# Optimization experiments

Measured on AMD Instinct MI355X. Metric: run time of the kernel, lower is better.

## Reference

```python
import jax, jax.numpy as jnp
from jax import lax
import numpy as np

BETA = 0.5       # leak factor of snn.Leaky
THR = 1.0        # firing threshold
SLOPE = 25.0     # fast_sigmoid surrogate slope (snntorch default)
NUM_STEPS = 16

@jax.custom_vjp
def spike(m):
    # Heaviside of (mem - threshold); surrogate grad = 1/(slope*|m|+1)^2
    return (m > 0).astype(m.dtype)

def _spike_fwd(m):
    return spike(m), m

def _spike_bwd(m, g):
    return (g / (SLOPE * jnp.abs(m) + 1.0) ** 2,)

spike.defvjp(_spike_fwd, _spike_bwd)


def setup_inputs() -> dict:
    key = jax.random.key(0)
    k1, k2, k3 = jax.random.split(key, 3)
    x = jax.random.uniform(k1, (4096, 1, 28, 28), dtype=jnp.float32)
    conv_w = jax.random.normal(k2, (8, 1, 3, 3), dtype=jnp.float32) * 0.3
    fc_w = jax.random.normal(k3, (10, 1352), dtype=jnp.float32) * 0.05
    return {"x": x, "conv_w": conv_w, "fc_w": fc_w}


def reference(x, conv_w, fc_w):
    B = x.shape[0]
    # conv1(x) is identical every timestep -> compute once (same math).
    cur1 = lax.conv_general_dilated(
        x, conv_w, window_strides=(1, 1), padding='VALID',
        dimension_numbers=('NCHW', 'OIHW', 'NCHW'))  # [B,8,26,26]

    mem1_0 = jnp.zeros_like(cur1)
    mem2_0 = jnp.zeros((B, 10), dtype=x.dtype)

    def step(carry, _):
        mem1, mem2 = carry
        # LIF layer 1: integrate, fire, subtract-reset (reset detached)
        mem1 = BETA * mem1 + cur1
        spk1 = spike(mem1 - THR)
        mem1 = mem1 - lax.stop_gradient(spk1) * THR
        # avg pool 2x2 -> [B,8,13,13]
        pool = spk1.reshape(B, 8, 13, 2, 13, 2).mean(axis=(3, 5))
        # fc (no bias): [B,1352] @ [1352,10]
        cur2 = pool.reshape(B, -1) @ fc_w.T
        # LIF layer 2
        mem2 = BETA * mem2 + cur2
        spk2 = spike(mem2 - THR)
        mem2 = mem2 - lax.stop_gradient(spk2) * THR
        return (mem1, mem2), spk2

    (_, _), spk2_rec = lax.scan(step, (mem1_0, mem2_0), None, length=NUM_STEPS)
    return spk2_rec.sum(axis=0)  # [B,10] spike counts
```

## Files before the change

### kernel.cpp

```cpp
#include <hip/hip_runtime.h>


typedef float v2f __attribute__((ext_vector_type(2)));
typedef unsigned v2u __attribute__((ext_vector_type(2)));

#if __has_builtin(__builtin_elementwise_fma)
#define VFMA(a, b, c) __builtin_elementwise_fma((a), (b), (c))
#else
#define VFMA(a, b, c) ((a) * (b) + (c))
#endif

#define NU 6

__device__ __forceinline__ float bfly16(float x) {
#if __has_builtin(__builtin_amdgcn_permlane16_swap)
    v2u r = __builtin_amdgcn_permlane16_swap(__float_as_uint(x), __float_as_uint(x),
                                             false, false);
    return __uint_as_float(r.x) + __uint_as_float(r.y);
#else
    return x + __shfl_xor(x, 16);
#endif
}

__device__ __forceinline__ float pairfold16(float a, float b) {
#if __has_builtin(__builtin_amdgcn_permlane16_swap)
    v2u r = __builtin_amdgcn_permlane16_swap(__float_as_uint(a), __float_as_uint(b),
                                             false, false);
    return __uint_as_float(r.x) + __uint_as_float(r.y);
#else
    const float sa = a + __shfl_xor(a, 16);
    const float sb = b + __shfl_xor(b, 16);
    return ((threadIdx.x & 16) != 0) ? sb : sa;
#endif
}

__device__ __forceinline__ float pairfold32(float a, float b) {
#if __has_builtin(__builtin_amdgcn_permlane32_swap)
    v2u r = __builtin_amdgcn_permlane32_swap(__float_as_uint(a), __float_as_uint(b),
                                             false, false);
    return __uint_as_float(r.x) + __uint_as_float(r.y);
#else
    const float sa = a + __shfl_xor(a, 32);
    const float sb = b + __shfl_xor(b, 32);
    return ((threadIdx.x & 32) != 0) ? sb : sa;
#endif
}

template<int N>
__device__ __forceinline__ float dpp_ror_add(float x) {
#if __has_builtin(__builtin_amdgcn_update_dpp)
    int y = __builtin_amdgcn_update_dpp(0, __float_as_int(x), 0x120 + N, 0xf, 0xf, false);
    return x + __int_as_float(y);
#else
    return x + __shfl_xor(x, N);
#endif
}

__global__ __launch_bounds__(256, 3) void snn_fused_kernel(
    const float* __restrict__ x,
    const float* __restrict__ conv_w,
    const float* __restrict__ fc_w,
    float* __restrict__ out)
{
    const int b    = blockIdx.x;
    const int tid  = threadIdx.x;
    const int lane = tid & 63;
    const int wid  = tid >> 6;

    __shared__ float scw[72];
    __shared__ float sred[16 * 165];
    __shared__ float scur2[160];

    if (tid < 72) scw[tid] = conv_w[tid];

    int xbase[NU], kbase[NU];
    v2f wl[NU][5];
    #pragma unroll
    for (int i = 0; i < NU; ++i) {
        const int u      = tid + 256 * i;
        const bool valid = (u < 1352);
        const int uu  = valid ? u : 0;
        const int k   = uu / 169;
        const int rem = uu - k * 169;
        const int pr  = rem / 13;
        const int pc  = rem - pr * 13;
        xbase[i] = 56 * pr + 2 * pc;
        kbase[i] = 9 * k;
        const float sc = valid ? 0.25f : 0.0f;
        #pragma unroll
        for (int j = 0; j < 5; ++j)
            wl[i][j] = (v2f){sc * fc_w[(2 * j) * 1352 + uu],
                             sc * fc_w[(2 * j + 1) * 1352 + uu]};
    }
    __syncthreads();

    const float* xb = x + (size_t)b * 784;
    v2f cur2[NU][2];
    v2f mem2[NU][2];
    #pragma unroll
    for (int i = 0; i < NU; ++i) {
        float cw[9];
        #pragma unroll
        for (int qq = 0; qq < 9; ++qq) cw[qq] = scw[kbase[i] + qq];

        float xr[4][4];
        #pragma unroll
        for (int r = 0; r < 4; ++r) {
            const float2* rp = reinterpret_cast<const float2*>(xb + xbase[i] + 28 * r);
            const float2 a = rp[0], c2 = rp[1];
            xr[r][0] = a.x; xr[r][1] = a.y; xr[r][2] = c2.x; xr[r][3] = c2.y;
        }

        const bool valid = (tid + 256 * i) < 1352;
        float cell[2][2];
        #pragma unroll
        for (int dr = 0; dr < 2; ++dr)
            #pragma unroll
            for (int dc = 0; dc < 2; ++dc) {
                float acc = 0.0f;
                #pragma unroll
                for (int ki = 0; ki < 3; ++ki)
                    #pragma unroll
                    for (int kj = 0; kj < 3; ++kj)
                        acc += xr[dr + ki][dc + kj] * cw[ki * 3 + kj];
                cell[dr][dc] = valid ? acc : 0.0f;
            }
        cur2[i][0] = (v2f){cell[0][0], cell[0][1]};
        cur2[i][1] = (v2f){cell[1][0], cell[1][1]};
        mem2[i][0] = (v2f){0.0f, 0.0f};
        mem2[i][1] = (v2f){0.0f, 0.0f};
    }

    const v2f half2 = (v2f){0.5f, 0.5f};

    auto stageA = [&](v2f& a01, v2f& a23, v2f& a45, v2f& a67, v2f& a89) {
        a01 = a23 = a45 = a67 = a89 = (v2f){0.0f, 0.0f};
        #pragma unroll
        for (int i = 0; i < NU; ++i) {
            v2f m01 = VFMA(half2, mem2[i][0], cur2[i][0]);
            v2f m23 = VFMA(half2, mem2[i][1], cur2[i][1]);
            v2f sp01, sp23;
            sp01.x = m01.x > 1.0f ? 1.0f : 0.0f;
            sp01.y = m01.y > 1.0f ? 1.0f : 0.0f;
            sp23.x = m23.x > 1.0f ? 1.0f : 0.0f;
            sp23.y = m23.y > 1.0f ? 1.0f : 0.0f;
            mem2[i][0] = m01 - sp01;
            mem2[i][1] = m23 - sp23;
            v2f s = sp01 + sp23;
            const float c = s.x + s.y;
            const v2f f2 = (v2f){c, c};
            a01 = VFMA(wl[i][0], f2, a01);
            a23 = VFMA(wl[i][1], f2, a23);
            a45 = VFMA(wl[i][2], f2, a45);
            a67 = VFMA(wl[i][3], f2, a67);
            a89 = VFMA(wl[i][4], f2, a89);
        }
    };

    v2f v01, v23, v45, v67, v89;
    stageA(v01, v23, v45, v67, v89);

    const int q   = lane >> 4;
    const int bo  = (q & 1) * 2 + (q >> 1) * 5;
    const int to  = 4 + (q >> 1) * 5;
    const int row = wid * 4 + (lane & 3);

    #pragma unroll
    for (int t = 0; t < 16; ++t) {
        const float s0 = pairfold32(v01.x, v45.y);
        const float s1 = pairfold32(v01.y, v67.x);
        const float s2 = pairfold32(v23.x, v67.y);
        const float s3 = pairfold32(v23.y, v89.x);
        const float s4 = pairfold32(v45.x, v89.y);
        float w0 = pairfold16(s0, s2);
        float w1 = pairfold16(s1, s3);
        float w2 = bfly16(s4);

        v2f n01, n23, n45, n67, n89;
        if (t < 15) {
            stageA(n01, n23, n45, n67, n89);
        } else {
            n01 = n23 = n45 = n67 = n89 = (v2f){0.0f, 0.0f};
        }

        w0 = dpp_ror_add<8>(w0);
        w1 = dpp_ror_add<8>(w1);
        w2 = dpp_ror_add<8>(w2);
        w0 = dpp_ror_add<4>(w0);
        w1 = dpp_ror_add<4>(w1);
        w2 = dpp_ror_add<4>(w2);

        if ((lane & 12) == 0) {
            const int base = row * 165 + t * 10;
            sred[base + bo]     = w0;
            sred[base + bo + 1] = w1;
            sred[base + to]     = w2;
        }

        v01 = n01; v23 = n23; v45 = n45; v67 = n67; v89 = n89;
    }
    __syncthreads();

    if (tid < 160) {
        float sum = 0.0f;
        #pragma unroll
        for (int r = 0; r < 16; ++r)
            sum += sred[r * 165 + tid];
        scur2[tid] = sum;
    }
    __syncthreads();

    if (tid < 10) {
        float m2 = 0.0f, cnt = 0.0f;
        #pragma unroll
        for (int t = 0; t < 16; ++t) {
            m2 = __builtin_fmaf(0.5f, m2, scur2[t * 10 + tid]);
            float ms = m2 - 1.0f;
            bool  sp = ms > 0.0f;
            m2  = sp ? ms : m2;
            cnt += sp ? 1.0f : 0.0f;
        }
        out[(size_t)b * 10 + tid] = cnt;
    }
}

extern "C" void kernel_launch(void* const* d_in, const int* in_sizes, int n_in,
                              void* d_out, int out_size, void* d_ws, size_t ws_size,
                              hipStream_t stream) {
    const float* x      = (const float*)d_in[0];
    const float* conv_w = (const float*)d_in[1];
    const float* fc_w   = (const float*)d_in[2];
    float* out          = (float*)d_out;

    const int B = in_sizes[0] / 784;
    snn_fused_kernel<<<B, 256, 0, stream>>>(x, conv_w, fc_w, out);
}
```

Before: 89.19 us.

## Compute FC layer with bf16 MFMA using split-precision weight fragments

```diff
diff --git a/kernel.cpp b/kernel.cpp
--- a/kernel.cpp
+++ b/kernel.cpp
@@ -2,7 +2,8 @@
 
 
 typedef float v2f __attribute__((ext_vector_type(2)));
-typedef unsigned v2u __attribute__((ext_vector_type(2)));
+typedef float f32x4 __attribute__((ext_vector_type(4)));
+typedef short s16x8 __attribute__((ext_vector_type(8)));
 
 #if __has_builtin(__builtin_elementwise_fma)
 #define VFMA(a, b, c) __builtin_elementwise_fma((a), (b), (c))
@@ -11,55 +12,43 @@
 #endif
 
 #define NU 6
+#define KS 43
+#define SPLITS 4
 
-__device__ __forceinline__ float bfly16(float x) {
-#if __has_builtin(__builtin_amdgcn_permlane16_swap)
-    v2u r = __builtin_amdgcn_permlane16_swap(__float_as_uint(x), __float_as_uint(x),
-                                             false, false);
-    return __uint_as_float(r.x) + __uint_as_float(r.y);
-#else
-    return x + __shfl_xor(x, 16);
-#endif
+__device__ __forceinline__ unsigned short bf16_rne(float f) {
+    unsigned u = __float_as_uint(f);
+    return (unsigned short)((u + 0x7FFFu + ((u >> 16) & 1u)) >> 16);
+}
+__device__ __forceinline__ float bf16_back(unsigned short h) {
+    return __uint_as_float(((unsigned)h) << 16);
 }
 
-__device__ __forceinline__ float pairfold16(float a, float b) {
-#if __has_builtin(__builtin_amdgcn_permlane16_swap)
-    v2u r = __builtin_amdgcn_permlane16_swap(__float_as_uint(a), __float_as_uint(b),
-                                             false, false);
-    return __uint_as_float(r.x) + __uint_as_float(r.y);
-#else
-    const float sa = a + __shfl_xor(a, 16);
-    const float sb = b + __shfl_xor(b, 16);
-    return ((threadIdx.x & 16) != 0) ? sb : sa;
-#endif
-}
-
-__device__ __forceinline__ float pairfold32(float a, float b) {
-#if __has_builtin(__builtin_amdgcn_permlane32_swap)
-    v2u r = __builtin_amdgcn_permlane32_swap(__float_as_uint(a), __float_as_uint(b),
-                                             false, false);
-    return __uint_as_float(r.x) + __uint_as_float(r.y);
-#else
-    const float sa = a + __shfl_xor(a, 32);
-    const float sb = b + __shfl_xor(b, 32);
-    return ((threadIdx.x & 32) != 0) ? sb : sa;
-#endif
-}
-
-template<int N>
-__device__ __forceinline__ float dpp_ror_add(float x) {
-#if __has_builtin(__builtin_amdgcn_update_dpp)
-    int y = __builtin_amdgcn_update_dpp(0, __float_as_int(x), 0x120 + N, 0xf, 0xf, false);
-    return x + __int_as_float(y);
-#else
-    return x + __shfl_xor(x, N);
-#endif
+__global__ void build_bfrag_kernel(const float* __restrict__ fc_w,
+                                   s16x8* __restrict__ wsfrag) {
+    const int blk = blockIdx.x;
+    const int p   = blk / KS;
+    const int ks  = blk - p * KS;
+    const int l   = threadIdx.x;
+    s16x8 frag;
+    #pragma unroll
+    for (int jj = 0; jj < 8; ++jj) {
+        const int k = ks * 32 + (l >> 4) * 8 + jj;
+        const int n = l & 15;
+        float r = (k < 1352 && n < 10) ? 0.25f * fc_w[n * 1352 + k] : 0.0f;
+        unsigned short b = 0;
+        for (int q = 0; q <= p; ++q) {
+            b = bf16_rne(r);
+            r -= bf16_back(b);
+        }
+        frag[jj] = (short)b;
+    }
+    wsfrag[blk * 64 + l] = frag;
 }
 
 __global__ __launch_bounds__(256, 3) void snn_fused_kernel(
     const float* __restrict__ x,
     const float* __restrict__ conv_w,
-    const float* __restrict__ fc_w,
+    const s16x8* __restrict__ wsfrag,
     float* __restrict__ out)
 {
     const int b    = blockIdx.x;
@@ -67,14 +56,13 @@
     const int lane = tid & 63;
     const int wid  = tid >> 6;
 
+    __shared__ unsigned short sA[KS * 544];
     __shared__ float scw[72];
-    __shared__ float sred[16 * 165];
     __shared__ float scur2[160];
 
     if (tid < 72) scw[tid] = conv_w[tid];
 
-    int xbase[NU], kbase[NU];
-    v2f wl[NU][5];
+    int xbase[NU], kbase[NU], sbase[NU];
     #pragma unroll
     for (int i = 0; i < NU; ++i) {
         const int u      = tid + 256 * i;
@@ -86,11 +74,8 @@
         const int pc  = rem - pr * 13;
         xbase[i] = 56 * pr + 2 * pc;
         kbase[i] = 9 * k;
-        const float sc = valid ? 0.25f : 0.0f;
-        #pragma unroll
-        for (int j = 0; j < 5; ++j)
-            wl[i][j] = (v2f){sc * fc_w[(2 * j) * 1352 + uu],
-                             sc * fc_w[(2 * j + 1) * 1352 + uu]};
+        const int uo = u & 31;
+        sbase[i] = (u >> 5) * 544 + (uo >> 3) * 136 + (uo & 7);
     }
     __syncthreads();
 
@@ -133,8 +118,8 @@
 
     const v2f half2 = (v2f){0.5f, 0.5f};
 
-    auto stageA = [&](v2f& a01, v2f& a23, v2f& a45, v2f& a67, v2f& a89) {
-        a01 = a23 = a45 = a67 = a89 = (v2f){0.0f, 0.0f};
+    #pragma unroll
+    for (int t = 0; t < 16; ++t) {
         #pragma unroll
         for (int i = 0; i < NU; ++i) {
             v2f m01 = VFMA(half2, mem2[i][0], cur2[i][0]);
@@ -148,65 +133,36 @@
             mem2[i][1] = m23 - sp23;
             v2f s = sp01 + sp23;
             const float c = s.x + s.y;
-            const v2f f2 = (v2f){c, c};
-            a01 = VFMA(wl[i][0], f2, a01);
-            a23 = VFMA(wl[i][1], f2, a23);
-            a45 = VFMA(wl[i][2], f2, a45);
-            a67 = VFMA(wl[i][3], f2, a67);
-            a89 = VFMA(wl[i][4], f2, a89);
+            const unsigned short cb = (unsigned short)(__float_as_uint(c) >> 16);
+            if (i < 5 || tid < 96)
+                sA[sbase[i] + t * 8] = cb;
         }
-    };
-
-    v2f v01, v23, v45, v67, v89;
-    stageA(v01, v23, v45, v67, v89);
-
-    const int q   = lane >> 4;
-    const int bo  = (q & 1) * 2 + (q >> 1) * 5;
-    const int to  = 4 + (q >> 1) * 5;
-    const int row = wid * 4 + (lane & 3);
-
-    #pragma unroll
-    for (int t = 0; t < 16; ++t) {
-        const float s0 = pairfold32(v01.x, v45.y);
-        const float s1 = pairfold32(v01.y, v67.x);
-        const float s2 = pairfold32(v23.x, v67.y);
-        const float s3 = pairfold32(v23.y, v89.x);
-        const float s4 = pairfold32(v45.x, v89.y);
-        float w0 = pairfold16(s0, s2);
-        float w1 = pairfold16(s1, s3);
-        float w2 = bfly16(s4);
-
-        v2f n01, n23, n45, n67, n89;
-        if (t < 15) {
-            stageA(n01, n23, n45, n67, n89);
-        } else {
-            n01 = n23 = n45 = n67 = n89 = (v2f){0.0f, 0.0f};
-        }
-
-        w0 = dpp_ror_add<8>(w0);
-        w1 = dpp_ror_add<8>(w1);
-        w2 = dpp_ror_add<8>(w2);
-        w0 = dpp_ror_add<4>(w0);
-        w1 = dpp_ror_add<4>(w1);
-        w2 = dpp_ror_add<4>(w2);
-
-        if ((lane & 12) == 0) {
-            const int base = row * 165 + t * 10;
-            sred[base + bo]     = w0;
-            sred[base + bo + 1] = w1;
-            sred[base + to]     = w2;
-        }
-
-        v01 = n01; v23 = n23; v45 = n45; v67 = n67; v89 = n89;
     }
     __syncthreads();
 
-    if (tid < 160) {
-        float sum = 0.0f;
+    if (wid == 0) {
+        f32x4 acc[SPLITS];
         #pragma unroll
-        for (int r = 0; r < 16; ++r)
-            sum += sred[r * 165 + tid];
-        scur2[tid] = sum;
+        for (int p = 0; p < SPLITS; ++p) acc[p] = (f32x4){0.f, 0.f, 0.f, 0.f};
+
+        const int arow = (lane >> 4) * 136 + (lane & 15) * 8;
+        for (int ks = 0; ks < KS; ++ks) {
+            const s16x8 a = *reinterpret_cast<const s16x8*>(&sA[ks * 544 + arow]);
+            #pragma unroll
+            for (int p = 0; p < SPLITS; ++p) {
+                const s16x8 bw = wsfrag[(p * KS + ks) * 64 + lane];
+                acc[p] = __builtin_amdgcn_mfma_f32_16x16x32_bf16(a, bw, acc[p], 0, 0, 0);
+            }
+        }
+        const f32x4 csum = (acc[0] + acc[1]) + (acc[2] + acc[3]);
+        const int o = lane & 15;
+        if (o < 10) {
+            #pragma unroll
+            for (int r = 0; r < 4; ++r) {
+                const int t = (lane >> 4) * 4 + r;
+                scur2[t * 10 + o] = csum[r];
+            }
+        }
     }
     __syncthreads();
 
@@ -231,7 +187,10 @@
     const float* conv_w = (const float*)d_in[1];
     const float* fc_w   = (const float*)d_in[2];
     float* out          = (float*)d_out;
+    s16x8* wsfrag       = (s16x8*)d_ws;
+
+    build_bfrag_kernel<<<SPLITS * KS, 64, 0, stream>>>(fc_w, wsfrag);
 
     const int B = in_sizes[0] / 784;
-    snn_fused_kernel<<<B, 256, 0, stream>>>(x, conv_w, fc_w, out);
+    snn_fused_kernel<<<B, 256, 0, stream>>>(x, conv_w, wsfrag, out);
 }
```

Result: slower. 135.5 us (+52.0%).
